# Performance work log

Hardware: AMD Instinct MI355X
Metric: run time of the kernel (lower is better)

The kernel has to match this reference:

```python
import jax, jax.numpy as jnp
import numpy as np

# dims
B, T, D, H, A = 256, 64, 6400, 1000, 4
# config['snn'] / config['adaptive_threshold'] values
BETA = 0.9          # 1 - voltage_decay(0.1)
THRESH = 1.0        # threshold_voltage
REST = 0.0          # resting_voltage
THETA_PLUS = 0.05
THETA_DECAY = 0.9


def setup_inputs() -> dict:
    key = jax.random.key(0)
    ks = jax.random.split(key, 7)
    x = jax.random.normal(ks[0], (B, T, D), jnp.float32)
    W1 = jax.random.normal(ks[1], (H, D), jnp.float32) * (1.0 / np.sqrt(D))
    b1 = jax.random.normal(ks[2], (H,), jnp.float32) * 0.01
    W2 = jax.random.normal(ks[3], (A, H), jnp.float32) * (1.0 / np.sqrt(H))
    b2 = jax.random.normal(ks[4], (A,), jnp.float32) * 0.01
    # pre-drawn uniforms for bernoulli sampling at each timestep/layer
    u1 = jax.random.uniform(ks[5], (T, B, H), jnp.float32)
    u2 = jax.random.uniform(ks[6], (T, B, A), jnp.float32)
    return {"x": x, "W1": W1, "b1": b1, "W2": W2, "b2": b2, "u1": u1, "u2": u2}


def _lif(cur, mem, theta, u):
    # StochasticAdaptiveLIF.forward
    mem = BETA * (mem - REST) + REST + cur
    prob = jax.nn.sigmoid(mem - (THRESH + theta))
    spk = (u < prob).astype(mem.dtype)  # bernoulli(prob)
    mem = mem * (1.0 - spk)
    theta = THETA_DECAY * theta + THETA_PLUS * spk
    return spk, mem, theta


def reference(x, W1, b1, W2, b2, u1, u2):
    xT = jnp.swapaxes(x, 0, 1)  # [T, B, D]

    def step(carry, inp):
        mem1, theta1, mem2, theta2 = carry
        xt, u1t, u2t = inp
        cur1 = xt @ W1.T + b1                      # [B, H]
        spk1, mem1, theta1 = _lif(cur1, mem1, theta1, u1t)
        cur2 = spk1 @ W2.T + b2                    # [B, A]
        spk2, mem2, theta2 = _lif(cur2, mem2, theta2, u2t)
        return (mem1, theta1, mem2, theta2), spk2

    init = (jnp.zeros((B, H), x.dtype), jnp.zeros((B, H), x.dtype),
            jnp.zeros((B, A), x.dtype), jnp.zeros((B, A), x.dtype))
    _, spks = jax.lax.scan(step, init, (xT, u1, u2))  # spks: [T, B, A]
    return spks.sum(0) / T
```

## Files before the change

### kernel.cpp

```cpp
#include <hip/hip_runtime.h>
#include <math.h>

#define B_  256
#define T_  64
#define D_  6400
#define H_  1000
#define A_  4

#define BM 256
#define BN 128
#define BK 16

typedef float v2f __attribute__((ext_vector_type(2)));

__device__ __forceinline__ void pk_fma(v2f& acc, float a, v2f b) {
  v2f as = {a, a};
  acc = __builtin_elementwise_fma(as, b, acc);
}

#define LGKM_BARRIER()                                         \
  do {                                                         \
    asm volatile("s_waitcnt lgkmcnt(0)" ::: "memory");         \
    __builtin_amdgcn_s_barrier();                              \
  } while (0)

__global__ __launch_bounds__(256, 2) void gemm1_kernel(
    const float* __restrict__ x, const float* __restrict__ W1,
    const float* __restrict__ b1, float* __restrict__ C1) {
  __shared__ float As[2][BK][BM + 4];
  __shared__ float Bs[2][BK][BN + 4];

  const int tid = threadIdx.x;
  const int m0 = blockIdx.y * BM;
  const int n0 = blockIdx.x * BN;
  const int tx = tid & 15;
  const int ty = tid >> 4;

  const int row = tid >> 2;
  const int col4 = tid & 3;

  v2f acc2[16][4];
#pragma unroll
  for (int i = 0; i < 16; ++i)
#pragma unroll
    for (int j = 0; j < 4; ++j) acc2[i][j] = (v2f){0.f, 0.f};

  float4 av[4], bv[2];

#define LOAD_TILE(kn)                                                         \
  do {                                                                        \
    if ((kn) < D_) {                                                          \
      _Pragma("unroll") for (int i = 0; i < 4; ++i) av[i] =                   \
          *(const float4*)(x + (size_t)(m0 + row + 64 * i) * D_ + (kn) +     \
                           col4 * 4);                                         \
      _Pragma("unroll") for (int i = 0; i < 2; ++i) {                         \
        const int hh = n0 + row + 64 * i;                                     \
        bv[i] = (hh < H_)                                                     \
                    ? *(const float4*)(W1 + (size_t)hh * D_ + (kn) +         \
                                       col4 * 4)                              \
                    : make_float4(0.f, 0.f, 0.f, 0.f);                        \
      }                                                                       \
    }                                                                         \
  } while (0)

#define STORE_TILE(bufi)                                                      \
  do {                                                                        \
    _Pragma("unroll") for (int i = 0; i < 4; ++i) {                           \
      const int r = row + 64 * i;                                             \
      As[bufi][col4 * 4 + 0][r] = av[i].x;                                    \
      As[bufi][col4 * 4 + 1][r] = av[i].y;                                    \
      As[bufi][col4 * 4 + 2][r] = av[i].z;                                    \
      As[bufi][col4 * 4 + 3][r] = av[i].w;                                    \
    }                                                                         \
    _Pragma("unroll") for (int i = 0; i < 2; ++i) {                           \
      const int r = row + 64 * i;                                             \
      Bs[bufi][col4 * 4 + 0][r] = bv[i].x;                                    \
      Bs[bufi][col4 * 4 + 1][r] = bv[i].y;                                    \
      Bs[bufi][col4 * 4 + 2][r] = bv[i].z;                                    \
      Bs[bufi][col4 * 4 + 3][r] = bv[i].w;                                    \
    }                                                                         \
  } while (0)

  LOAD_TILE(0);
  STORE_TILE(0);
  LOAD_TILE(BK);
  LGKM_BARRIER();

  int cur = 0;
  for (int k0 = 0; k0 < D_; k0 += BK) {
    const int nxt = cur ^ 1;
    if (k0 + BK < D_) {
      STORE_TILE(nxt);
      LOAD_TILE(k0 + 2 * BK);
    }
#pragma unroll
    for (int k = 0; k < BK; ++k) {
      const float4 a0 = *(const float4*)&As[cur][k][ty * 4];
      const float4 a1 = *(const float4*)&As[cur][k][64 + ty * 4];
      const float4 a2 = *(const float4*)&As[cur][k][128 + ty * 4];
      const float4 a3 = *(const float4*)&As[cur][k][192 + ty * 4];
      const float4 b0 = *(const float4*)&Bs[cur][k][tx * 4];
      const float4 b1v = *(const float4*)&Bs[cur][k][64 + tx * 4];
      v2f bp[4] = {{b0.x, b0.y}, {b0.z, b0.w}, {b1v.x, b1v.y}, {b1v.z, b1v.w}};
      const float as_[16] = {a0.x, a0.y, a0.z, a0.w, a1.x, a1.y, a1.z, a1.w,
                             a2.x, a2.y, a2.z, a2.w, a3.x, a3.y, a3.z, a3.w};
#pragma unroll
      for (int f = 0; f < 16; ++f) {
#pragma unroll
        for (int j = 0; j < 4; ++j) {
          pk_fma(acc2[f][j], as_[f], bp[j]);
        }
      }
    }
    LGKM_BARRIER();
    cur = nxt;
  }

  const int h0 = n0 + tx * 4;
  const int h1 = n0 + 64 + tx * 4;
  float4 bias0 = (h0 < H_) ? *(const float4*)(b1 + h0)
                           : make_float4(0.f, 0.f, 0.f, 0.f);
  float4 bias1 = (h1 < H_) ? *(const float4*)(b1 + h1)
                           : make_float4(0.f, 0.f, 0.f, 0.f);
#pragma unroll
  for (int f = 0; f < 16; ++f) {
    const int m = m0 + 64 * (f >> 2) + ty * 4 + (f & 3);
    const int bb = m >> 6;
    const int tt = m & 63;
    float* op = C1 + (size_t)tt * (B_ * H_) + (size_t)bb * H_;
    if (h0 < H_) {
      float4 r;
      r.x = acc2[f][0].x + bias0.x;
      r.y = acc2[f][0].y + bias0.y;
      r.z = acc2[f][1].x + bias0.z;
      r.w = acc2[f][1].y + bias0.w;
      *(float4*)(op + h0) = r;
    }
    if (h1 < H_) {
      float4 r;
      r.x = acc2[f][2].x + bias1.x;
      r.y = acc2[f][2].y + bias1.y;
      r.z = acc2[f][3].x + bias1.z;
      r.w = acc2[f][3].y + bias1.w;
      *(float4*)(op + h1) = r;
    }
  }
#undef LOAD_TILE
#undef STORE_TILE
}

__device__ __forceinline__ float sigmoid_f(float z) {
  return 1.0f / (1.0f + expf(-z));
}

__global__ __launch_bounds__(256) void snn_seq_kernel(
    const float* __restrict__ C1, const float* __restrict__ u1,
    const float* __restrict__ W2, const float* __restrict__ b2,
    const float* __restrict__ u2, float* __restrict__ out) {
  const int b = blockIdx.x;
  const int tid = threadIdx.x;
  const int lane = tid & 63;
  const int wv = tid >> 6;

  __shared__ float sRed[2][4][A_];
  __shared__ float sU2[T_ * A_];

  sU2[tid] = u2[(size_t)(tid >> 2) * (B_ * A_) + (size_t)b * A_ + (tid & 3)];

  const bool act = (tid < 250);
  const int h = tid * 4;

  float wreg[A_][4];
#pragma unroll
  for (int a = 0; a < A_; ++a)
#pragma unroll
    for (int j = 0; j < 4; ++j) wreg[a][j] = 0.f;
  if (act) {
#pragma unroll
    for (int a = 0; a < A_; ++a) {
      const float4 w = *(const float4*)(W2 + (size_t)a * H_ + h);
      wreg[a][0] = w.x;
      wreg[a][1] = w.y;
      wreg[a][2] = w.z;
      wreg[a][3] = w.w;
    }
  }
  const float b2v = (tid < A_) ? b2[tid] : 0.f;

  __syncthreads();

  float mem1v[4] = {0.f, 0.f, 0.f, 0.f};
  float th1v[4] = {0.f, 0.f, 0.f, 0.f};
  float mem2v = 0.f, th2v = 0.f, scnt = 0.f;

  float4 c_cur = make_float4(0.f, 0.f, 0.f, 0.f);
  float4 u_cur = make_float4(0.f, 0.f, 0.f, 0.f);
  if (act) {
    c_cur = *(const float4*)(C1 + (size_t)b * H_ + h);
    u_cur = *(const float4*)(u1 + (size_t)b * H_ + h);
  }

  for (int t = 0; t < T_; ++t) {
    float4 c_nxt = make_float4(0.f, 0.f, 0.f, 0.f);
    float4 u_nxt = make_float4(0.f, 0.f, 0.f, 0.f);
    if (act && (t + 1 < T_)) {
      const size_t off = ((size_t)(t + 1) * B_ + b) * H_ + h;
      c_nxt = *(const float4*)(C1 + off);
      u_nxt = *(const float4*)(u1 + off);
    }

    float part0 = 0.f, part1 = 0.f, part2 = 0.f, part3 = 0.f;
    if (act) {
      const float cs[4] = {c_cur.x, c_cur.y, c_cur.z, c_cur.w};
      const float us[4] = {u_cur.x, u_cur.y, u_cur.z, u_cur.w};
#pragma unroll
      for (int j = 0; j < 4; ++j) {
        float m = fmaf(0.9f, mem1v[j], cs[j]);
        const float z = m - (1.0f + th1v[j]);
        const float p = sigmoid_f(z);
        const float spk = (us[j] < p) ? 1.0f : 0.0f;
        m = (spk != 0.0f) ? 0.0f : m;
        th1v[j] = fmaf(0.9f, th1v[j], 0.05f * spk);
        mem1v[j] = m;
        part0 = fmaf(spk, wreg[0][j], part0);
        part1 = fmaf(spk, wreg[1][j], part1);
        part2 = fmaf(spk, wreg[2][j], part2);
        part3 = fmaf(spk, wreg[3][j], part3);
      }
    }

#pragma unroll
    for (int off = 32; off >= 1; off >>= 1) {
      part0 += __shfl_down(part0, off);
      part1 += __shfl_down(part1, off);
      part2 += __shfl_down(part2, off);
      part3 += __shfl_down(part3, off);
    }
    if (lane == 0) {
      float* r = &sRed[t & 1][wv][0];
      r[0] = part0;
      r[1] = part1;
      r[2] = part2;
      r[3] = part3;
    }
    __syncthreads();

    if (tid < A_) {
      const int a = tid;
      const float cur2 = sRed[t & 1][0][a] + sRed[t & 1][1][a] +
                         sRed[t & 1][2][a] + sRed[t & 1][3][a] + b2v;
      float m = fmaf(0.9f, mem2v, cur2);
      const float z = m - (1.0f + th2v);
      const float p = sigmoid_f(z);
      const float u = sU2[t * A_ + a];
      const float spk = (u < p) ? 1.0f : 0.0f;
      mem2v = (spk != 0.0f) ? 0.0f : m;
      th2v = fmaf(0.9f, th2v, 0.05f * spk);
      scnt += spk;
    }

    c_cur = c_nxt;
    u_cur = u_nxt;
  }

  if (tid < A_) out[b * A_ + tid] = scnt * (1.0f / 64.0f);
}

extern "C" void kernel_launch(void* const* d_in, const int* in_sizes, int n_in,
                              void* d_out, int out_size, void* d_ws,
                              size_t ws_size, hipStream_t stream) {
  const float* x = (const float*)d_in[0];
  const float* W1 = (const float*)d_in[1];
  const float* b1 = (const float*)d_in[2];
  const float* W2 = (const float*)d_in[3];
  const float* b2 = (const float*)d_in[4];
  const float* u1 = (const float*)d_in[5];
  const float* u2 = (const float*)d_in[6];
  float* out = (float*)d_out;
  float* C1 = (float*)d_ws;

  dim3 g1((H_ + BN - 1) / BN, (B_ * T_) / BM);
  gemm1_kernel<<<g1, 256, 0, stream>>>(x, W1, b1, C1);
  snn_seq_kernel<<<B_, 256, 0, stream>>>(C1, u1, W2, b2, u2, out);
}
```

Baseline: 2.960 ms.

## Split GEMM tile across 512 threads and run SNN recurrence in one wave

```diff
diff --git a/kernel.cpp b/kernel.cpp
--- a/kernel.cpp
+++ b/kernel.cpp
@@ -11,20 +11,13 @@
 #define BN 128
 #define BK 16
 
-typedef float v2f __attribute__((ext_vector_type(2)));
-
-__device__ __forceinline__ void pk_fma(v2f& acc, float a, v2f b) {
-  v2f as = {a, a};
-  acc = __builtin_elementwise_fma(as, b, acc);
-}
-
 #define LGKM_BARRIER()                                         \
   do {                                                         \
     asm volatile("s_waitcnt lgkmcnt(0)" ::: "memory");         \
     __builtin_amdgcn_s_barrier();                              \
   } while (0)
 
-__global__ __launch_bounds__(256, 2) void gemm1_kernel(
+__global__ __launch_bounds__(512, 4) void gemm1_kernel(
     const float* __restrict__ x, const float* __restrict__ W1,
     const float* __restrict__ b1, float* __restrict__ C1) {
   __shared__ float As[2][BK][BM + 4];
@@ -33,52 +26,48 @@
   const int tid = threadIdx.x;
   const int m0 = blockIdx.y * BM;
   const int n0 = blockIdx.x * BN;
-  const int tx = tid & 15;
-  const int ty = tid >> 4;
-
-  const int row = tid >> 2;
+  const int tx = tid & 31;
+  const int ty = tid >> 5;
+
+  const int row_a = tid >> 2;
   const int col4 = tid & 3;
 
-  v2f acc2[16][4];
-#pragma unroll
-  for (int i = 0; i < 16; ++i)
-#pragma unroll
-    for (int j = 0; j < 4; ++j) acc2[i][j] = (v2f){0.f, 0.f};
-
-  float4 av[4], bv[2];
+  float acc[16][4];
+#pragma unroll
+  for (int f = 0; f < 16; ++f)
+#pragma unroll
+    for (int c = 0; c < 4; ++c) acc[f][c] = 0.f;
+
+  float4 av0, av1, bv;
 
 #define LOAD_TILE(kn)                                                         \
   do {                                                                        \
     if ((kn) < D_) {                                                          \
-      _Pragma("unroll") for (int i = 0; i < 4; ++i) av[i] =                   \
-          *(const float4*)(x + (size_t)(m0 + row + 64 * i) * D_ + (kn) +     \
-                           col4 * 4);                                         \
-      _Pragma("unroll") for (int i = 0; i < 2; ++i) {                         \
-        const int hh = n0 + row + 64 * i;                                     \
-        bv[i] = (hh < H_)                                                     \
-                    ? *(const float4*)(W1 + (size_t)hh * D_ + (kn) +         \
-                                       col4 * 4)                              \
-                    : make_float4(0.f, 0.f, 0.f, 0.f);                        \
-      }                                                                       \
+      av0 = *(const float4*)(x + (size_t)(m0 + row_a) * D_ + (kn) +          \
+                             col4 * 4);                                       \
+      av1 = *(const float4*)(x + (size_t)(m0 + row_a + 128) * D_ + (kn) +    \
+                             col4 * 4);                                       \
+      const int hh = n0 + row_a;                                              \
+      bv = (hh < H_) ? *(const float4*)(W1 + (size_t)hh * D_ + (kn) +        \
+                                        col4 * 4)                             \
+                     : make_float4(0.f, 0.f, 0.f, 0.f);                       \
     }                                                                         \
   } while (0)
 
 #define STORE_TILE(bufi)                                                      \
   do {                                                                        \
-    _Pragma("unroll") for (int i = 0; i < 4; ++i) {                           \
-      const int r = row + 64 * i;                                             \
-      As[bufi][col4 * 4 + 0][r] = av[i].x;                                    \
-      As[bufi][col4 * 4 + 1][r] = av[i].y;                                    \
-      As[bufi][col4 * 4 + 2][r] = av[i].z;                                    \
-      As[bufi][col4 * 4 + 3][r] = av[i].w;                                    \
-    }                                                                         \
-    _Pragma("unroll") for (int i = 0; i < 2; ++i) {                           \
-      const int r = row + 64 * i;                                             \
-      Bs[bufi][col4 * 4 + 0][r] = bv[i].x;                                    \
-      Bs[bufi][col4 * 4 + 1][r] = bv[i].y;                                    \
-      Bs[bufi][col4 * 4 + 2][r] = bv[i].z;                                    \
-      Bs[bufi][col4 * 4 + 3][r] = bv[i].w;                                    \
-    }                                                                         \
+    As[bufi][col4 * 4 + 0][row_a] = av0.x;                                    \
+    As[bufi][col4 * 4 + 1][row_a] = av0.y;                                    \
+    As[bufi][col4 * 4 + 2][row_a] = av0.z;                                    \
+    As[bufi][col4 * 4 + 3][row_a] = av0.w;                                    \
+    As[bufi][col4 * 4 + 0][row_a + 128] = av1.x;                              \
+    As[bufi][col4 * 4 + 1][row_a + 128] = av1.y;                              \
+    As[bufi][col4 * 4 + 2][row_a + 128] = av1.z;                              \
+    As[bufi][col4 * 4 + 3][row_a + 128] = av1.w;                              \
+    Bs[bufi][col4 * 4 + 0][row_a] = bv.x;                                     \
+    Bs[bufi][col4 * 4 + 1][row_a] = bv.y;                                     \
+    Bs[bufi][col4 * 4 + 2][row_a] = bv.z;                                     \
+    Bs[bufi][col4 * 4 + 3][row_a] = bv.w;                                     \
   } while (0)
 
   LOAD_TILE(0);
@@ -99,16 +88,15 @@
       const float4 a1 = *(const float4*)&As[cur][k][64 + ty * 4];
       const float4 a2 = *(const float4*)&As[cur][k][128 + ty * 4];
       const float4 a3 = *(const float4*)&As[cur][k][192 + ty * 4];
-      const float4 b0 = *(const float4*)&Bs[cur][k][tx * 4];
-      const float4 b1v = *(const float4*)&Bs[cur][k][64 + tx * 4];
-      v2f bp[4] = {{b0.x, b0.y}, {b0.z, b0.w}, {b1v.x, b1v.y}, {b1v.z, b1v.w}};
-      const float as_[16] = {a0.x, a0.y, a0.z, a0.w, a1.x, a1.y, a1.z, a1.w,
-                             a2.x, a2.y, a2.z, a2.w, a3.x, a3.y, a3.z, a3.w};
+      const float4 b = *(const float4*)&Bs[cur][k][tx * 4];
+      const float am[16] = {a0.x, a0.y, a0.z, a0.w, a1.x, a1.y, a1.z, a1.w,
+                            a2.x, a2.y, a2.z, a2.w, a3.x, a3.y, a3.z, a3.w};
+      const float bc[4] = {b.x, b.y, b.z, b.w};
 #pragma unroll
       for (int f = 0; f < 16; ++f) {
 #pragma unroll
-        for (int j = 0; j < 4; ++j) {
-          pk_fma(acc2[f][j], as_[f], bp[j]);
+        for (int c = 0; c < 4; ++c) {
+          acc[f][c] = fmaf(am[f], bc[c], acc[f][c]);
         }
       }
     }
@@ -117,32 +105,20 @@
   }
 
   const int h0 = n0 + tx * 4;
-  const int h1 = n0 + 64 + tx * 4;
-  float4 bias0 = (h0 < H_) ? *(const float4*)(b1 + h0)
-                           : make_float4(0.f, 0.f, 0.f, 0.f);
-  float4 bias1 = (h1 < H_) ? *(const float4*)(b1 + h1)
-                           : make_float4(0.f, 0.f, 0.f, 0.f);
+  float4 bias = (h0 < H_) ? *(const float4*)(b1 + h0)
+                          : make_float4(0.f, 0.f, 0.f, 0.f);
 #pragma unroll
   for (int f = 0; f < 16; ++f) {
     const int m = m0 + 64 * (f >> 2) + ty * 4 + (f & 3);
     const int bb = m >> 6;
     const int tt = m & 63;
-    float* op = C1 + (size_t)tt * (B_ * H_) + (size_t)bb * H_;
     if (h0 < H_) {
       float4 r;
-      r.x = acc2[f][0].x + bias0.x;
-      r.y = acc2[f][0].y + bias0.y;
-      r.z = acc2[f][1].x + bias0.z;
-      r.w = acc2[f][1].y + bias0.w;
-      *(float4*)(op + h0) = r;
-    }
-    if (h1 < H_) {
-      float4 r;
-      r.x = acc2[f][2].x + bias1.x;
-      r.y = acc2[f][2].y + bias1.y;
-      r.z = acc2[f][3].x + bias1.z;
-      r.w = acc2[f][3].y + bias1.w;
-      *(float4*)(op + h1) = r;
+      r.x = acc[f][0] + bias.x;
+      r.y = acc[f][1] + bias.y;
+      r.z = acc[f][2] + bias.z;
+      r.w = acc[f][3] + bias.w;
+      *(float4*)(C1 + (size_t)tt * (B_ * H_) + (size_t)bb * H_ + h0) = r;
     }
   }
 #undef LOAD_TILE
@@ -153,117 +129,136 @@
   return 1.0f / (1.0f + expf(-z));
 }
 
-__global__ __launch_bounds__(256) void snn_seq_kernel(
+__global__ __launch_bounds__(64) void snn_seq_kernel(
     const float* __restrict__ C1, const float* __restrict__ u1,
     const float* __restrict__ W2, const float* __restrict__ b2,
     const float* __restrict__ u2, float* __restrict__ out) {
   const int b = blockIdx.x;
-  const int tid = threadIdx.x;
-  const int lane = tid & 63;
-  const int wv = tid >> 6;
-
-  __shared__ float sRed[2][4][A_];
-  __shared__ float sU2[T_ * A_];
-
-  sU2[tid] = u2[(size_t)(tid >> 2) * (B_ * A_) + (size_t)b * A_ + (tid & 3)];
-
-  const bool act = (tid < 250);
-  const int h = tid * 4;
-
-  float wreg[A_][4];
+  const int l = threadIdx.x;
+
+  float wreg[A_][4][4];
 #pragma unroll
   for (int a = 0; a < A_; ++a)
 #pragma unroll
-    for (int j = 0; j < 4; ++j) wreg[a][j] = 0.f;
-  if (act) {
-#pragma unroll
-    for (int a = 0; a < A_; ++a) {
-      const float4 w = *(const float4*)(W2 + (size_t)a * H_ + h);
-      wreg[a][0] = w.x;
-      wreg[a][1] = w.y;
-      wreg[a][2] = w.z;
-      wreg[a][3] = w.w;
-    }
-  }
-  const float b2v = (tid < A_) ? b2[tid] : 0.f;
-
-  __syncthreads();
-
-  float mem1v[4] = {0.f, 0.f, 0.f, 0.f};
-  float th1v[4] = {0.f, 0.f, 0.f, 0.f};
-  float mem2v = 0.f, th2v = 0.f, scnt = 0.f;
-
-  float4 c_cur = make_float4(0.f, 0.f, 0.f, 0.f);
-  float4 u_cur = make_float4(0.f, 0.f, 0.f, 0.f);
-  if (act) {
-    c_cur = *(const float4*)(C1 + (size_t)b * H_ + h);
-    u_cur = *(const float4*)(u1 + (size_t)b * H_ + h);
-  }
+    for (int jj = 0; jj < 4; ++jj) {
+      const int h = jj * 256 + l * 4;
+      float4 w = (h < H_) ? *(const float4*)(W2 + (size_t)a * H_ + h)
+                          : make_float4(0.f, 0.f, 0.f, 0.f);
+      wreg[a][jj][0] = w.x;
+      wreg[a][jj][1] = w.y;
+      wreg[a][jj][2] = w.z;
+      wreg[a][jj][3] = w.w;
+    }
+  const float4 b2v = *(const float4*)b2;
+
+  float mem1[4][4], th1[4][4];
+#pragma unroll
+  for (int jj = 0; jj < 4; ++jj)
+#pragma unroll
+    for (int e = 0; e < 4; ++e) {
+      mem1[jj][e] = 0.f;
+      th1[jj][e] = 0.f;
+    }
+  float mem2[A_] = {0.f, 0.f, 0.f, 0.f};
+  float th2[A_] = {0.f, 0.f, 0.f, 0.f};
+  float scnt[A_] = {0.f, 0.f, 0.f, 0.f};
+
+  float4 c_cur[4], u_cur[4];
+#pragma unroll
+  for (int jj = 0; jj < 4; ++jj) {
+    const int h = jj * 256 + l * 4;
+    if (h < H_) {
+      const size_t off = (size_t)b * H_ + h;
+      c_cur[jj] = *(const float4*)(C1 + off);
+      u_cur[jj] = *(const float4*)(u1 + off);
+    } else {
+      c_cur[jj] = make_float4(0.f, 0.f, 0.f, 0.f);
+      u_cur[jj] = make_float4(2.f, 2.f, 2.f, 2.f);
+    }
+  }
+  float4 u2c = *(const float4*)(u2 + (size_t)b * A_);
 
   for (int t = 0; t < T_; ++t) {
-    float4 c_nxt = make_float4(0.f, 0.f, 0.f, 0.f);
-    float4 u_nxt = make_float4(0.f, 0.f, 0.f, 0.f);
-    if (act && (t + 1 < T_)) {
-      const size_t off = ((size_t)(t + 1) * B_ + b) * H_ + h;
-      c_nxt = *(const float4*)(C1 + off);
-      u_nxt = *(const float4*)(u1 + off);
-    }
-
-    float part0 = 0.f, part1 = 0.f, part2 = 0.f, part3 = 0.f;
-    if (act) {
-      const float cs[4] = {c_cur.x, c_cur.y, c_cur.z, c_cur.w};
-      const float us[4] = {u_cur.x, u_cur.y, u_cur.z, u_cur.w};
-#pragma unroll
-      for (int j = 0; j < 4; ++j) {
-        float m = fmaf(0.9f, mem1v[j], cs[j]);
-        const float z = m - (1.0f + th1v[j]);
+    float4 c_nxt[4], u_nxt[4], u2n;
+#pragma unroll
+    for (int jj = 0; jj < 4; ++jj) {
+      c_nxt[jj] = make_float4(0.f, 0.f, 0.f, 0.f);
+      u_nxt[jj] = make_float4(2.f, 2.f, 2.f, 2.f);
+    }
+    u2n = make_float4(0.f, 0.f, 0.f, 0.f);
+    if (t + 1 < T_) {
+#pragma unroll
+      for (int jj = 0; jj < 4; ++jj) {
+        const int h = jj * 256 + l * 4;
+        if (h < H_) {
+          const size_t off = ((size_t)(t + 1) * B_ + b) * H_ + h;
+          c_nxt[jj] = *(const float4*)(C1 + off);
+          u_nxt[jj] = *(const float4*)(u1 + off);
+        }
+      }
+      u2n = *(const float4*)(u2 + ((size_t)(t + 1) * B_ + b) * A_);
+    }
+
+    float p0 = 0.f, p1 = 0.f, p2 = 0.f, p3 = 0.f;
+#pragma unroll
+    for (int jj = 0; jj < 4; ++jj) {
+      const float cs[4] = {c_cur[jj].x, c_cur[jj].y, c_cur[jj].z, c_cur[jj].w};
+      const float us[4] = {u_cur[jj].x, u_cur[jj].y, u_cur[jj].z, u_cur[jj].w};
+#pragma unroll
+      for (int e = 0; e < 4; ++e) {
+        float m = fmaf(0.9f, mem1[jj][e], cs[e]);
+        const float z = m - (1.0f + th1[jj][e]);
         const float p = sigmoid_f(z);
-        const float spk = (us[j] < p) ? 1.0f : 0.0f;
+        const float spk = (us[e] < p) ? 1.0f : 0.0f;
         m = (spk != 0.0f) ? 0.0f : m;
-        th1v[j] = fmaf(0.9f, th1v[j], 0.05f * spk);
-        mem1v[j] = m;
-        part0 = fmaf(spk, wreg[0][j], part0);
-        part1 = fmaf(spk, wreg[1][j], part1);
-        part2 = fmaf(spk, wreg[2][j], part2);
-        part3 = fmaf(spk, wreg[3][j], part3);
+        th1[jj][e] = fmaf(0.9f, th1[jj][e], 0.05f * spk);
+        mem1[jj][e] = m;
+        p0 = fmaf(spk, wreg[0][jj][e], p0);
+        p1 = fmaf(spk, wreg[1][jj][e], p1);
+        p2 = fmaf(spk, wreg[2][jj][e], p2);
+        p3 = fmaf(spk, wreg[3][jj][e], p3);
       }
     }
 
 #pragma unroll
     for (int off = 32; off >= 1; off >>= 1) {
-      part0 += __shfl_down(part0, off);
-      part1 += __shfl_down(part1, off);
-      part2 += __shfl_down(part2, off);
-      part3 += __shfl_down(part3, off);
-    }
-    if (lane == 0) {
-      float* r = &sRed[t & 1][wv][0];
-      r[0] = part0;
-      r[1] = part1;
-      r[2] = part2;
-      r[3] = part3;
-    }
-    __syncthreads();
-
-    if (tid < A_) {
-      const int a = tid;
-      const float cur2 = sRed[t & 1][0][a] + sRed[t & 1][1][a] +
-                         sRed[t & 1][2][a] + sRed[t & 1][3][a] + b2v;
-      float m = fmaf(0.9f, mem2v, cur2);
-      const float z = m - (1.0f + th2v);
-      const float p = sigmoid_f(z);
-      const float u = sU2[t * A_ + a];
-      const float spk = (u < p) ? 1.0f : 0.0f;
-      mem2v = (spk != 0.0f) ? 0.0f : m;
-      th2v = fmaf(0.9f, th2v, 0.05f * spk);
-      scnt += spk;
-    }
-
-    c_cur = c_nxt;
-    u_cur = u_nxt;
-  }
-
-  if (tid < A_) out[b * A_ + tid] = scnt * (1.0f / 64.0f);
+      p0 += __shfl_down(p0, off);
+      p1 += __shfl_down(p1, off);
+      p2 += __shfl_down(p2, off);
+      p3 += __shfl_down(p3, off);
+    }
+
+    if (l == 0) {
+      const float cur2[4] = {p0 + b2v.x, p1 + b2v.y, p2 + b2v.z, p3 + b2v.w};
+      const float uu[4] = {u2c.x, u2c.y, u2c.z, u2c.w};
+#pragma unroll
+      for (int a = 0; a < A_; ++a) {
+        float m = fmaf(0.9f, mem2[a], cur2[a]);
+        const float z = m - (1.0f + th2[a]);
+        const float p = sigmoid_f(z);
+        const float spk = (uu[a] < p) ? 1.0f : 0.0f;
+        mem2[a] = (spk != 0.0f) ? 0.0f : m;
+        th2[a] = fmaf(0.9f, th2[a], 0.05f * spk);
+        scnt[a] += spk;
+      }
+    }
+
+#pragma unroll
+    for (int jj = 0; jj < 4; ++jj) {
+      c_cur[jj] = c_nxt[jj];
+      u_cur[jj] = u_nxt[jj];
+    }
+    u2c = u2n;
+  }
+
+  if (l == 0) {
+    float4 r;
+    r.x = scnt[0] * (1.0f / 64.0f);
+    r.y = scnt[1] * (1.0f / 64.0f);
+    r.z = scnt[2] * (1.0f / 64.0f);
+    r.w = scnt[3] * (1.0f / 64.0f);
+    *(float4*)(out + (size_t)b * A_) = r;
+  }
 }
 
 extern "C" void kernel_launch(void* const* d_in, const int* in_sizes, int n_in,
@@ -280,6 +275,6 @@
   float* C1 = (float*)d_ws;
 
   dim3 g1((H_ + BN - 1) / BN, (B_ * T_) / BM);
-  gemm1_kernel<<<g1, 256, 0, stream>>>(x, W1, b1, C1);
-  snn_seq_kernel<<<B_, 256, 0, stream>>>(C1, u1, W2, b2, u2, out);
-}
+  gemm1_kernel<<<g1, 512, 0, stream>>>(x, W1, b1, C1);
+  snn_seq_kernel<<<B_, 64, 0, stream>>>(C1, u1, W2, b2, u2, out);
+}
```

New measurement: 3.699 ms. +25.0%, slower.
